# Kernel optimization log

Measured on AMD Instinct MI355X. Metric: run time of the kernel, lower is better.

The kernel has to match this reference:

```python
import jax, jax.numpy as jnp
import numpy as np

N = 100000      # num nodes
E = 1600000     # num edges
NFEAT = 512
NHID = 256
NCLASS = 32
K = 10
ALPHA = 0.1


def setup_inputs() -> dict:
    key = jax.random.key(0)
    ks = jax.random.split(key, 6)
    x = jax.random.normal(ks[0], (N, NFEAT), dtype=jnp.float32)
    edge_index = jax.random.randint(ks[1], (2, E), 0, N, dtype=jnp.int32)
    edge_attr = jax.random.uniform(ks[2], (E,), dtype=jnp.float32)
    # Linear params (Kaiming-ish scale)
    W_start = jax.random.normal(ks[3], (NFEAT, NHID), dtype=jnp.float32) * np.float32(1.0 / np.sqrt(NFEAT))
    b_start = jnp.zeros((NHID,), jnp.float32)
    W_end = jax.random.normal(ks[4], (NHID, NCLASS), dtype=jnp.float32) * np.float32(1.0 / np.sqrt(NHID))
    b_end = jnp.zeros((NCLASS,), jnp.float32)
    # GPR 'PPR' init coefficients: temp[k] = alpha*(1-alpha)^k, temp[K] = (1-alpha)^K
    temp = (ALPHA * (1.0 - ALPHA) ** np.arange(K + 1)).astype(np.float32)
    temp[-1] = np.float32((1.0 - ALPHA) ** K)
    temp = jnp.asarray(temp)
    return {"x": x, "edge_attr": edge_attr, "W_start": W_start, "b_start": b_start,
            "W_end": W_end, "b_end": b_end, "temp": temp, "edge_index": edge_index}


def gcn_norm(edge_index, edge_weight, num_nodes):
    # add self loops with weight 1 (PyG default fill_value=1)
    loop = jnp.arange(num_nodes, dtype=edge_index.dtype)
    ei = jnp.concatenate([edge_index, jnp.stack([loop, loop])], axis=1)   # [2, E+N]
    ew = jnp.concatenate([edge_weight, jnp.ones((num_nodes,), edge_weight.dtype)])
    row, col = ei[0], ei[1]
    deg = jax.ops.segment_sum(ew, col, num_segments=num_nodes)            # [N]
    dis = jnp.where(deg > 0, jax.lax.rsqrt(jnp.where(deg > 0, deg, 1.0)), 0.0)
    norm = dis[row] * ew * dis[col]                                       # [E+N]
    return ei, norm


def reference(x, edge_attr, W_start, b_start, W_end, b_end, temp, edge_index):
    # MLP front-end (eval mode: dropout is identity)
    h = jax.nn.relu(x @ W_start + b_start)        # [N, NHID]
    h = jax.nn.relu(h @ W_end + b_end)            # [N, NCLASS]
    ei, norm = gcn_norm(edge_index, edge_attr, N)
    row, col = ei[0], ei[1]
    hidden = h * temp[0]
    xk = h
    for k in range(K):
        # SpMM: gather messages norm * x[row], scatter-add at col
        xk = jax.ops.segment_sum(norm[:, None] * xk[row], col, num_segments=N)
        hidden = hidden + temp[k + 1] * xk
    return hidden
```

## Files before the change

### kernel.cpp

```cpp
#include <hip/hip_runtime.h>

typedef __attribute__((ext_vector_type(8))) short short8;
typedef __attribute__((ext_vector_type(4))) float f32x4;
typedef unsigned long long u64;

constexpr int NN = 100000;
constexpr int EE = 1600000;
constexpr int NF = 512;
constexpr int NH = 256;
constexpr int NC = 32;
constexpr int KP = 10;

__device__ __forceinline__ unsigned short f2bf(float f) {
  unsigned int u = __float_as_uint(f);
  u += 0x7FFFu + ((u >> 16) & 1u);
  return (unsigned short)(u >> 16);
}
__device__ __forceinline__ float bf2f(unsigned short s) {
  return __uint_as_float(((unsigned int)s) << 16);
}
__device__ __forceinline__ int padc(int c) { return (c + 15) & ~15; }

__device__ __forceinline__ short8 cvt8(float4 a0, float4 a1) {
  union { unsigned int u[4]; short8 s; } r;
  asm("v_cvt_pk_bf16_f32 %0, %1, %2" : "=v"(r.u[0]) : "v"(a0.x), "v"(a0.y));
  asm("v_cvt_pk_bf16_f32 %0, %1, %2" : "=v"(r.u[1]) : "v"(a0.z), "v"(a0.w));
  asm("v_cvt_pk_bf16_f32 %0, %1, %2" : "=v"(r.u[2]) : "v"(a1.x), "v"(a1.y));
  asm("v_cvt_pk_bf16_f32 %0, %1, %2" : "=v"(r.u[3]) : "v"(a1.z), "v"(a1.w));
  return r.s;
}

__device__ __forceinline__ void block_sync_lds() {
  asm volatile("s_waitcnt lgkmcnt(0)" ::: "memory");
  __builtin_amdgcn_s_barrier();
}

__global__ void convwb_kernel(const float* __restrict__ Ws, const float* __restrict__ We,
                              unsigned short* __restrict__ Wt, unsigned short* __restrict__ Web) {
  int idx = blockIdx.x * 256 + threadIdx.x;
  if (idx < 131072) {
    int col = idx >> 9, k = idx & 511;
    Wt[idx] = f2bf(Ws[(size_t)k * NH + col]);
  } else {
    int j = idx - 131072;
    int col = j >> 8, k = j & 255;
    Web[j] = f2bf(We[(size_t)k * NC + col]);
  }
}

__global__ __launch_bounds__(256, 3) void gemm1_kernel(
    const float* __restrict__ X, const unsigned short* __restrict__ Wt,
    const float* __restrict__ bias, unsigned short* __restrict__ H) {
  constexpr int PAD = 36;
  __shared__ __align__(16) unsigned short Asm[2][128 * PAD];
  __shared__ __align__(16) unsigned short Bsm[2][128 * PAD];
  const int tid = threadIdx.x;
  const int lane = tid & 63;
  const int wave = tid >> 6;
  const int wm = wave >> 1, wn = wave & 1;
  const int l15 = lane & 15, kq = lane >> 4;
  const int m0 = (blockIdx.x >> 1) * 128;
  const int n0 = (blockIdx.x & 1) * 128;

  const int arl0 = tid >> 2, aq = tid & 3;
  int ar0 = m0 + arl0; if (ar0 >= NN) ar0 = NN - 1;
  int ar1 = m0 + arl0 + 64; if (ar1 >= NN) ar1 = NN - 1;
  const float* aptr0 = X + (size_t)ar0 * NF + aq * 8;
  const float* aptr1 = X + (size_t)ar1 * NF + aq * 8;
  const int awr0 = arl0 * PAD + aq * 8;
  const int awr1 = awr0 + 64 * PAD;
  const int bcl = tid >> 1, bh = tid & 1;
  const unsigned short* bptr = Wt + (size_t)(n0 + bcl) * NF + bh * 16;
  const int bwr = bcl * PAD + bh * 16;

  f32x4 acc[4][4];
#pragma unroll
  for (int m = 0; m < 4; m++)
#pragma unroll
    for (int n = 0; n < 4; n++) acc[m][n] = (f32x4)0.0f;

  float4 ra[3][4]; short8 rb0[3], rb1[3];

#define LOADR(ks, j) do { \
    ra[j][0] = *reinterpret_cast<const float4*>(aptr0 + (ks) * 32); \
    ra[j][1] = *reinterpret_cast<const float4*>(aptr0 + (ks) * 32 + 4); \
    ra[j][2] = *reinterpret_cast<const float4*>(aptr1 + (ks) * 32); \
    ra[j][3] = *reinterpret_cast<const float4*>(aptr1 + (ks) * 32 + 4); \
    rb0[j] = *reinterpret_cast<const short8*>(bptr + (ks) * 32); \
    rb1[j] = *reinterpret_cast<const short8*>(bptr + (ks) * 32 + 8); \
  } while (0)

#define STAGE(b, j) do { \
    *reinterpret_cast<short8*>(&Asm[b][awr0]) = cvt8(ra[j][0], ra[j][1]); \
    *reinterpret_cast<short8*>(&Asm[b][awr1]) = cvt8(ra[j][2], ra[j][3]); \
    *reinterpret_cast<short8*>(&Bsm[b][bwr]) = rb0[j]; \
    *reinterpret_cast<short8*>(&Bsm[b][bwr + 8]) = rb1[j]; \
  } while (0)

#define COMPUTE(b) do { \
    short8 af[4], bfr[4]; \
    _Pragma("unroll") \
    for (int mi = 0; mi < 4; mi++) \
      af[mi] = *reinterpret_cast<const short8*>(&Asm[b][(wm * 64 + mi * 16 + l15) * PAD + kq * 8]); \
    _Pragma("unroll") \
    for (int ni = 0; ni < 4; ni++) \
      bfr[ni] = *reinterpret_cast<const short8*>(&Bsm[b][(wn * 64 + ni * 16 + l15) * PAD + kq * 8]); \
    _Pragma("unroll") \
    for (int mi = 0; mi < 4; mi++) \
      _Pragma("unroll") \
      for (int ni = 0; ni < 4; ni++) \
        acc[mi][ni] = __builtin_amdgcn_mfma_f32_16x16x32_bf16(af[mi], bfr[ni], acc[mi][ni], 0, 0, 0); \
  } while (0)

  LOADR(0, 0);
  LOADR(1, 1);
  LOADR(2, 2);
  STAGE(0, 0);
  block_sync_lds();

#pragma unroll
  for (int p = 0; p < 16; p++) {
    if (p + 3 < 16) LOADR(p + 3, (p + 3) % 3);
    COMPUTE(p & 1);
    if (p + 1 < 16) STAGE((p + 1) & 1, (p + 1) % 3);
    block_sync_lds();
  }
#undef LOADR
#undef STAGE
#undef COMPUTE

#pragma unroll
  for (int ni = 0; ni < 4; ni++) {
    int col = n0 + wn * 64 + ni * 16 + l15;
    float bsv = bias[col];
#pragma unroll
    for (int mi = 0; mi < 4; mi++) {
      int rb2 = m0 + wm * 64 + mi * 16 + kq * 4;
#pragma unroll
      for (int i = 0; i < 4; i++) {
        int r = rb2 + i;
        if (r < NN) {
          float v = acc[mi][ni][i] + bsv;
          H[(size_t)r * NH + col] = f2bf(v > 0.f ? v : 0.f);
        }
      }
    }
  }
}

__global__ __launch_bounds__(256) void gemm2_kernel(
    const unsigned short* __restrict__ H, const unsigned short* __restrict__ Web,
    const float* __restrict__ be, const float* __restrict__ temp,
    unsigned short* __restrict__ x0b, float* __restrict__ out) {
  const int tid = threadIdx.x;
  const int lane = tid & 63;
  const int wave = tid >> 6;
  const int l15 = lane & 15, kq = lane >> 4;
  const int rbase = blockIdx.x * 64 + wave * 16;
  int rr = rbase + l15; if (rr >= NN) rr = NN - 1;
  const unsigned short* hrow = H + (size_t)rr * NH + kq * 8;
  const unsigned short* wrow = Web + (size_t)l15 * 256 + kq * 8;

  f32x4 acc[2];
  acc[0] = (f32x4)0.0f; acc[1] = (f32x4)0.0f;
#pragma unroll
  for (int ks = 0; ks < 8; ks++) {
    short8 a = *reinterpret_cast<const short8*>(hrow + ks * 32);
    short8 b0 = *reinterpret_cast<const short8*>(wrow + ks * 32);
    short8 b1 = *reinterpret_cast<const short8*>(wrow + 16 * 256 + ks * 32);
    acc[0] = __builtin_amdgcn_mfma_f32_16x16x32_bf16(a, b0, acc[0], 0, 0, 0);
    acc[1] = __builtin_amdgcn_mfma_f32_16x16x32_bf16(a, b1, acc[1], 0, 0, 0);
  }
  const float t0 = temp[0];
#pragma unroll
  for (int nt = 0; nt < 2; nt++) {
    int col = nt * 16 + l15;
    float bv = be[col];
#pragma unroll
    for (int i = 0; i < 4; i++) {
      int row = rbase + kq * 4 + i;
      if (row < NN) {
        float v = acc[nt][i] + bv;
        v = v > 0.f ? v : 0.f;
        x0b[(size_t)row * NC + col] = f2bf(v);
        out[(size_t)row * NC + col] = t0 * v;
      }
    }
  }
}

__global__ void node_init_kernel(u64* dc) {
  int i = blockIdx.x * 256 + threadIdx.x;
  if (i < NN) dc[i] = (1ULL << 44) | (1ULL << 32);
}

__global__ void edge_deg_kernel(const int* __restrict__ ei, const float* __restrict__ ew,
                                u64* dc) {
  int e = blockIdx.x * 256 + threadIdx.x;
  if (e < EE) {
    int col = ei[EE + e];
    u64 v = (1ULL << 44) | (u64)((double)ew[e] * 4294967296.0);
    atomicAdd(&dc[col], v);
  }
}

__global__ void dis_kernel(const u64* __restrict__ dc, float* __restrict__ dis,
                           int* __restrict__ cnt) {
  int i = blockIdx.x * 256 + threadIdx.x;
  if (i < NN) {
    u64 v = dc[i];
    cnt[i] = (int)(v >> 44);
    float deg = (float)((double)(v & 0xFFFFFFFFFFFULL) * (1.0 / 4294967296.0));
    dis[i] = rsqrtf(deg);
  }
}

__global__ void scan1_kernel(const int* __restrict__ cnt, int* bsum) {
  __shared__ int ws[4];
  const int tid = threadIdx.x;
  int base = blockIdx.x * 1024 + tid * 4;
  int s = 0;
#pragma unroll
  for (int j = 0; j < 4; j++) { int i = base + j; if (i < NN) s += padc(cnt[i]); }
  for (int off = 32; off > 0; off >>= 1) s += __shfl_down(s, off);
  if ((tid & 63) == 0) ws[tid >> 6] = s;
  __syncthreads();
  if (tid == 0) bsum[blockIdx.x] = ws[0] + ws[1] + ws[2] + ws[3];
}

__global__ void scan2_kernel(const int* __restrict__ bsum, int* bofs, int* offs) {
  if (threadIdx.x == 0) {
    int run = 0;
    for (int i = 0; i < 98; i++) { bofs[i] = run; run += bsum[i]; }
    offs[NN] = run;
  }
}

__global__ void scan3_kernel(const int* __restrict__ cnt, const int* __restrict__ bofs,
                             int* offs, int* cursor) {
  __shared__ int wsum[4];
  const int tid = threadIdx.x;
  const int lane = tid & 63, wv = tid >> 6;
  int base = blockIdx.x * 1024 + tid * 4;
  int v[4]; int s = 0;
#pragma unroll
  for (int j = 0; j < 4; j++) { int i = base + j; v[j] = (i < NN) ? padc(cnt[i]) : 0; s += v[j]; }
  int incl = s;
  for (int off = 1; off < 64; off <<= 1) {
    int t = __shfl_up(incl, off);
    if (lane >= off) incl += t;
  }
  if (lane == 63) wsum[wv] = incl;
  __syncthreads();
  int woff = bofs[blockIdx.x];
  for (int w = 0; w < wv; w++) woff += wsum[w];
  int excl = woff + incl - s;
#pragma unroll
  for (int j = 0; j < 4; j++) {
    int i = base + j;
    if (i < NN) { offs[i] = excl; cursor[i] = excl; }
    excl += v[j];
  }
}

__global__ void fill_kernel(const int* __restrict__ ei, const float* __restrict__ ew,
                            const float* __restrict__ dis, int* cursor,
                            u64* __restrict__ pk) {
  int t = blockIdx.x * 256 + threadIdx.x;
  if (t < EE) {
    int r = ei[t], c = ei[EE + t];
    int slot = atomicAdd(&cursor[c], 1);
    unsigned int wb = __float_as_uint(dis[r] * ew[t] * dis[c]);
    pk[slot] = (u64)(unsigned int)r | ((u64)wb << 32);
  } else if (t < EE + NN) {
    int i = t - EE;
    int slot = atomicAdd(&cursor[i], 1);
    float d = dis[i];
    unsigned int wb = __float_as_uint(d * d);
    pk[slot] = (u64)(unsigned int)i | ((u64)wb << 32);
  }
}

__global__ void pad_kernel(const int* __restrict__ cursor, const int* __restrict__ offs,
                           u64* __restrict__ pk) {
  int i = blockIdx.x * 256 + threadIdx.x;
  if (i < NN) {
    int j = cursor[i], e = offs[i + 1];
    for (; j < e; j++) pk[j] = 0;
  }
}

__global__ __launch_bounds__(256) void spmm_kernel(
    const int* __restrict__ offs, const u64* __restrict__ pk,
    const unsigned short* __restrict__ xin, unsigned short* __restrict__ xout) {
  const int tid = threadIdx.x;
  const int node = blockIdx.x * 64 + (tid >> 2);
  const int fo = (tid & 3) * 8;
  if (node >= NN) return;
  const int s = offs[node], e = offs[node + 1];
  float a[8];
#pragma unroll
  for (int t = 0; t < 8; t++) a[t] = 0.f;
  for (int j = s; j < e; j += 4) {
    ulonglong2 p01 = *reinterpret_cast<const ulonglong2*>(pk + j);
    ulonglong2 p23 = *reinterpret_cast<const ulonglong2*>(pk + j + 2);
    const u64 pa[4] = {p01.x, p01.y, p23.x, p23.y};
    short8 q[4];
#pragma unroll
    for (int i = 0; i < 4; i++)
      q[i] = *reinterpret_cast<const short8*>(xin + (size_t)(unsigned int)pa[i] * NC + fo);
#pragma unroll
    for (int i = 0; i < 4; i++) {
      const float w = __uint_as_float((unsigned int)(pa[i] >> 32));
#pragma unroll
      for (int t = 0; t < 8; t++)
        a[t] += w * bf2f((unsigned short)q[i][t]);
    }
  }
  union { unsigned int u[4]; short8 s8; } st;
  asm("v_cvt_pk_bf16_f32 %0, %1, %2" : "=v"(st.u[0]) : "v"(a[0]), "v"(a[1]));
  asm("v_cvt_pk_bf16_f32 %0, %1, %2" : "=v"(st.u[1]) : "v"(a[2]), "v"(a[3]));
  asm("v_cvt_pk_bf16_f32 %0, %1, %2" : "=v"(st.u[2]) : "v"(a[4]), "v"(a[5]));
  asm("v_cvt_pk_bf16_f32 %0, %1, %2" : "=v"(st.u[3]) : "v"(a[6]), "v"(a[7]));
  *reinterpret_cast<short8*>(xout + (size_t)node * NC + fo) = st.s8;
}

__global__ __launch_bounds__(256) void wsum_kernel(
    const unsigned short* __restrict__ S07,
    const unsigned short* __restrict__ S8, const unsigned short* __restrict__ S9,
    float* __restrict__ out, const float* __restrict__ temp) {
  int t8 = blockIdx.x * 256 + threadIdx.x;
  if (t8 >= NN * NC / 8) return;
  const size_t base = (size_t)t8 * 8;
  float s[8];
  float4 o0 = *reinterpret_cast<const float4*>(out + base);
  float4 o1 = *reinterpret_cast<const float4*>(out + base + 4);
  s[0] = o0.x; s[1] = o0.y; s[2] = o0.z; s[3] = o0.w;
  s[4] = o1.x; s[5] = o1.y; s[6] = o1.z; s[7] = o1.w;
#pragma unroll
  for (int k = 0; k < 8; k++) {
    const float tk = temp[k + 1];
    short8 v = *reinterpret_cast<const short8*>(S07 + (size_t)k * NN * NC + base);
#pragma unroll
    for (int t = 0; t < 8; t++) s[t] += tk * bf2f((unsigned short)v[t]);
  }
  {
    const float tk = temp[9];
    short8 v = *reinterpret_cast<const short8*>(S8 + base);
#pragma unroll
    for (int t = 0; t < 8; t++) s[t] += tk * bf2f((unsigned short)v[t]);
  }
  {
    const float tk = temp[10];
    short8 v = *reinterpret_cast<const short8*>(S9 + base);
#pragma unroll
    for (int t = 0; t < 8; t++) s[t] += tk * bf2f((unsigned short)v[t]);
  }
  *reinterpret_cast<float4*>(out + base) = make_float4(s[0], s[1], s[2], s[3]);
  *reinterpret_cast<float4*>(out + base + 4) = make_float4(s[4], s[5], s[6], s[7]);
}

extern "C" void kernel_launch(void* const* d_in, const int* in_sizes, int n_in,
                              void* d_out, int out_size, void* d_ws, size_t ws_size,
                              hipStream_t stream) {
  const float* X    = (const float*)d_in[0];
  const float* EA   = (const float*)d_in[1];
  const float* Ws   = (const float*)d_in[2];
  const float* bs   = (const float*)d_in[3];
  const float* We   = (const float*)d_in[4];
  const float* be   = (const float*)d_in[5];
  const float* temp = (const float*)d_in[6];
  const int*   ei   = (const int*)d_in[7];
  float* out = (float*)d_out;

  size_t off = 0;
  auto alloc = [&](size_t n) { void* p = (char*)d_ws + off; off += (n + 255) & ~(size_t)255; return p; };
  unsigned short* Wt  = (unsigned short*)alloc((size_t)NF * NH * 2);
  unsigned short* Web = (unsigned short*)alloc((size_t)NH * NC * 2);
  unsigned short* H   = (unsigned short*)alloc((size_t)NN * NH * 2);
  unsigned short* x0b = (unsigned short*)alloc((size_t)NN * NC * 2);
  unsigned short* xk8 = (unsigned short*)alloc((size_t)NN * NC * 2);
  unsigned short* xk9 = (unsigned short*)alloc((size_t)NN * NC * 2);
  u64*   dc   = (u64*)alloc((size_t)NN * 8);
  float* dis  = (float*)alloc((size_t)NN * 4);
  int*   cnt  = (int*)alloc((size_t)NN * 4);
  int*   offs = (int*)alloc((size_t)(NN + 1) * 4);
  int*   cursor = (int*)alloc((size_t)NN * 4);
  int*   bsum = (int*)alloc(98 * 4);
  int*   bofs = (int*)alloc(98 * 4);
  u64*   pk   = (u64*)alloc((size_t)(EE + 16 * NN) * 8);

  convwb_kernel<<<544, 256, 0, stream>>>(Ws, We, Wt, Web);
  gemm1_kernel<<<1564, 256, 0, stream>>>(X, Wt, bs, H);
  gemm2_kernel<<<1563, 256, 0, stream>>>(H, Web, be, temp, x0b, out);

  node_init_kernel<<<391, 256, 0, stream>>>(dc);
  edge_deg_kernel<<<6250, 256, 0, stream>>>(ei, EA, dc);
  dis_kernel<<<391, 256, 0, stream>>>(dc, dis, cnt);
  scan1_kernel<<<98, 256, 0, stream>>>(cnt, bsum);
  scan2_kernel<<<1, 64, 0, stream>>>(bsum, bofs, offs);
  scan3_kernel<<<98, 256, 0, stream>>>(cnt, bofs, offs, cursor);
  fill_kernel<<<6641, 256, 0, stream>>>(ei, EA, dis, cursor, pk);
  pad_kernel<<<391, 256, 0, stream>>>(cursor, offs, pk);

  auto slice = [&](int k) -> unsigned short* {
    return (k < 8) ? H + (size_t)k * NN * NC : (k == 8 ? xk8 : xk9);
  };
  const unsigned short* xin = x0b;
  for (int k = 0; k < KP; k++) {
    spmm_kernel<<<1563, 256, 0, stream>>>(offs, pk, xin, slice(k));
    xin = slice(k);
  }
  wsum_kernel<<<1563, 256, 0, stream>>>(H, xk8, xk9, out, temp);
}
```

Measured before the change: 589.5 us.

## Bucket nodes by padded degree and remap SpMM to 8 lanes per node

```diff
diff --git a/kernel.cpp b/kernel.cpp
--- a/kernel.cpp
+++ b/kernel.cpp
@@ -189,8 +189,9 @@
   }
 }
 
-__global__ void node_init_kernel(u64* dc) {
+__global__ void node_init_kernel(u64* dc, int* bcnt) {
   int i = blockIdx.x * 256 + threadIdx.x;
+  if (i < 64) bcnt[i] = 0;
   if (i < NN) dc[i] = (1ULL << 44) | (1ULL << 32);
 }
 
@@ -212,6 +213,30 @@
     cnt[i] = (int)(v >> 44);
     float deg = (float)((double)(v & 0xFFFFFFFFFFFULL) * (1.0 / 4294967296.0));
     dis[i] = rsqrtf(deg);
+  }
+}
+
+__global__ void bhist_kernel(const int* __restrict__ cnt, int* bcnt) {
+  int i = blockIdx.x * 256 + threadIdx.x;
+  if (i < NN) {
+    int b = padc(cnt[i]) >> 4; if (b > 63) b = 63;
+    atomicAdd(&bcnt[b], 1);
+  }
+}
+
+__global__ void bscan_kernel(const int* __restrict__ bcnt, int* bcur) {
+  if (threadIdx.x == 0) {
+    int run = 0;
+    for (int b = 0; b < 64; b++) { bcur[b] = run; run += bcnt[b]; }
+  }
+}
+
+__global__ void bscatter_kernel(const int* __restrict__ cnt, int* bcur,
+                                int* __restrict__ nidx) {
+  int i = blockIdx.x * 256 + threadIdx.x;
+  if (i < NN) {
+    int b = padc(cnt[i]) >> 4; if (b > 63) b = 63;
+    nidx[atomicAdd(&bcur[b], 1)] = i;
   }
 }
 
@@ -292,37 +317,38 @@
 
 __global__ __launch_bounds__(256) void spmm_kernel(
     const int* __restrict__ offs, const u64* __restrict__ pk,
+    const int* __restrict__ nidx,
     const unsigned short* __restrict__ xin, unsigned short* __restrict__ xout) {
   const int tid = threadIdx.x;
-  const int node = blockIdx.x * 64 + (tid >> 2);
-  const int fo = (tid & 3) * 8;
-  if (node >= NN) return;
+  const int ni = blockIdx.x * 32 + (tid >> 3);
+  const int fq = (tid & 7) * 4;
+  const int node = nidx[ni];
   const int s = offs[node], e = offs[node + 1];
-  float a[8];
-#pragma unroll
-  for (int t = 0; t < 8; t++) a[t] = 0.f;
-  for (int j = s; j < e; j += 4) {
+  float a0 = 0.f, a1 = 0.f, a2 = 0.f, a3 = 0.f;
+  for (int j = s; j < e; j += 8) {
     ulonglong2 p01 = *reinterpret_cast<const ulonglong2*>(pk + j);
     ulonglong2 p23 = *reinterpret_cast<const ulonglong2*>(pk + j + 2);
-    const u64 pa[4] = {p01.x, p01.y, p23.x, p23.y};
-    short8 q[4];
-#pragma unroll
-    for (int i = 0; i < 4; i++)
-      q[i] = *reinterpret_cast<const short8*>(xin + (size_t)(unsigned int)pa[i] * NC + fo);
-#pragma unroll
-    for (int i = 0; i < 4; i++) {
-      const float w = __uint_as_float((unsigned int)(pa[i] >> 32));
-#pragma unroll
-      for (int t = 0; t < 8; t++)
-        a[t] += w * bf2f((unsigned short)q[i][t]);
+    ulonglong2 p45 = *reinterpret_cast<const ulonglong2*>(pk + j + 4);
+    ulonglong2 p67 = *reinterpret_cast<const ulonglong2*>(pk + j + 6);
+    const u64 p[8] = {p01.x, p01.y, p23.x, p23.y, p45.x, p45.y, p67.x, p67.y};
+    u64 q[8];
+#pragma unroll
+    for (int i = 0; i < 8; i++)
+      q[i] = *reinterpret_cast<const u64*>(xin + (size_t)(unsigned int)p[i] * NC + fq);
+#pragma unroll
+    for (int i = 0; i < 8; i++) {
+      const float w = __uint_as_float((unsigned int)(p[i] >> 32));
+      a0 += w * bf2f((unsigned short)(q[i]));
+      a1 += w * bf2f((unsigned short)(q[i] >> 16));
+      a2 += w * bf2f((unsigned short)(q[i] >> 32));
+      a3 += w * bf2f((unsigned short)(q[i] >> 48));
     }
   }
-  union { unsigned int u[4]; short8 s8; } st;
-  asm("v_cvt_pk_bf16_f32 %0, %1, %2" : "=v"(st.u[0]) : "v"(a[0]), "v"(a[1]));
-  asm("v_cvt_pk_bf16_f32 %0, %1, %2" : "=v"(st.u[1]) : "v"(a[2]), "v"(a[3]));
-  asm("v_cvt_pk_bf16_f32 %0, %1, %2" : "=v"(st.u[2]) : "v"(a[4]), "v"(a[5]));
-  asm("v_cvt_pk_bf16_f32 %0, %1, %2" : "=v"(st.u[3]) : "v"(a[6]), "v"(a[7]));
-  *reinterpret_cast<short8*>(xout + (size_t)node * NC + fo) = st.s8;
+  unsigned int lo, hi;
+  asm("v_cvt_pk_bf16_f32 %0, %1, %2" : "=v"(lo) : "v"(a0), "v"(a1));
+  asm("v_cvt_pk_bf16_f32 %0, %1, %2" : "=v"(hi) : "v"(a2), "v"(a3));
+  *reinterpret_cast<u64*>(xout + (size_t)node * NC + fq) =
+      (u64)lo | ((u64)hi << 32);
 }
 
 __global__ __launch_bounds__(256) void wsum_kernel(
@@ -388,15 +414,21 @@
   int*   cursor = (int*)alloc((size_t)NN * 4);
   int*   bsum = (int*)alloc(98 * 4);
   int*   bofs = (int*)alloc(98 * 4);
+  int*   bcnt = (int*)alloc(64 * 4);
+  int*   bcur = (int*)alloc(64 * 4);
+  int*   nidx = (int*)alloc((size_t)NN * 4);
   u64*   pk   = (u64*)alloc((size_t)(EE + 16 * NN) * 8);
 
   convwb_kernel<<<544, 256, 0, stream>>>(Ws, We, Wt, Web);
   gemm1_kernel<<<1564, 256, 0, stream>>>(X, Wt, bs, H);
   gemm2_kernel<<<1563, 256, 0, stream>>>(H, Web, be, temp, x0b, out);
 
-  node_init_kernel<<<391, 256, 0, stream>>>(dc);
+  node_init_kernel<<<391, 256, 0, stream>>>(dc, bcnt);
   edge_deg_kernel<<<6250, 256, 0, stream>>>(ei, EA, dc);
   dis_kernel<<<391, 256, 0, stream>>>(dc, dis, cnt);
+  bhist_kernel<<<391, 256, 0, stream>>>(cnt, bcnt);
+  bscan_kernel<<<1, 64, 0, stream>>>(bcnt, bcur);
+  bscatter_kernel<<<391, 256, 0, stream>>>(cnt, bcur, nidx);
   scan1_kernel<<<98, 256, 0, stream>>>(cnt, bsum);
   scan2_kernel<<<1, 64, 0, stream>>>(bsum, bofs, offs);
   scan3_kernel<<<98, 256, 0, stream>>>(cnt, bofs, offs, cursor);
@@ -408,7 +440,7 @@
   };
   const unsigned short* xin = x0b;
   for (int k = 0; k < KP; k++) {
-    spmm_kernel<<<1563, 256, 0, stream>>>(offs, pk, xin, slice(k));
+    spmm_kernel<<<3125, 256, 0, stream>>>(offs, pk, nidx, xin, slice(k));
     xin = slice(k);
   }
   wsum_kernel<<<1563, 256, 0, stream>>>(H, xk8, xk9, out, temp);
```

Result: slower. 2.115 ms (+258.7%).
